# Kernel optimization log

Hardware: AMD Instinct MI355X
Metric: run time of the kernel (lower is better)

## Reference

```python
import jax, jax.numpy as jnp
import numpy as np

EMBED_DIM = 1024
NUM_HEADS = 8
HEAD_DIM = EMBED_DIM // NUM_HEADS


def setup_inputs() -> dict:
    key = jax.random.key(0)
    k1, k2, k3, k4, k5 = jax.random.split(key, 5)
    B, N, D = 4, 2048, EMBED_DIM
    scale = 1.0 / np.sqrt(D)
    return {
        "representation": jax.random.normal(k1, (B, N, D), dtype=jnp.float32),
        "W_qkv": jax.random.normal(k2, (D, 3 * D), dtype=jnp.float32) * scale,
        "b_qkv": jnp.zeros((3 * D,), dtype=jnp.float32),
        "W_proj": jax.random.normal(k3, (D, D), dtype=jnp.float32) * scale,
        "b_proj": jnp.zeros((D,), dtype=jnp.float32),
    }


def reference(representation, W_qkv, b_qkv, W_proj, b_proj):
    B, N, D = representation.shape
    H, Hd = NUM_HEADS, HEAD_DIM
    qkv = jnp.einsum("bnd,de->bne", representation, W_qkv) + b_qkv  # [B,N,3D]
    q, k, v = jnp.split(qkv, 3, axis=-1)
    # [B,N,D] -> [B,H,N,Hd]
    split_heads = lambda x: x.reshape(B, N, H, Hd).transpose(0, 2, 1, 3)
    q, k, v = split_heads(q), split_heads(k), split_heads(v)
    dots = jnp.einsum("bhqd,bhkd->bhqk", q, k) * (Hd ** -0.5)  # [B,H,N,N]
    attn = jax.nn.softmax(dots, axis=-1)
    out = jnp.einsum("bhqk,bhkd->bhqd", attn, v)
    out = out.transpose(0, 2, 1, 3).reshape(B, N, D)  # merge heads
    return jnp.einsum("bnd,de->bne", out, W_proj) + b_proj
```

## Files before the change

### kernel.cpp

```cpp
#include <hip/hip_runtime.h>
#include <hip/hip_bf16.h>
#include <cstdint>

typedef unsigned short u16;
typedef __attribute__((ext_vector_type(8))) short short8;
typedef __attribute__((ext_vector_type(4))) float f32x4;
typedef __attribute__((ext_vector_type(4))) unsigned short u16x4;

#define NSEQ 2048
#define DMODEL 1024
#define NH 8
#define HD 128
#define KDIM 1024
#define SCALE 0.08838834764831845f

__device__ __forceinline__ u16 f2b(float f) {
  __hip_bfloat16 h = __float2bfloat16(f);
  union { __hip_bfloat16 h; u16 u; } cv; cv.h = h; return cv.u;
}
__device__ __forceinline__ f32x4 zero4() { f32x4 z = {0.f, 0.f, 0.f, 0.f}; return z; }

__device__ __forceinline__ void gload_lds16(const u16* g, u16* l) {
  __builtin_amdgcn_global_load_lds(
      (__attribute__((address_space(1))) void*)g,
      (__attribute__((address_space(3))) void*)l, 16, 0, 0);
}

__global__ void cvt_f32_bf16(const float* __restrict__ in, u16* __restrict__ out) {
  const size_t i = ((size_t)blockIdx.x * 256 + threadIdx.x) * 8;
  f32x4 a = *(const f32x4*)&in[i];
  f32x4 b = *(const f32x4*)&in[i + 4];
  short8 o;
#pragma unroll
  for (int j = 0; j < 4; ++j) { o[j] = (short)f2b(a[j]); o[4 + j] = (short)f2b(b[j]); }
  *(short8*)&out[i] = o;
}

__global__ void transpose_k(const float* __restrict__ in, u16* __restrict__ out,
                            int R, int C) {
  __shared__ u16 tile[32][33];
  const int tx = threadIdx.x, ty = threadIdx.y;
  const int c = blockIdx.x * 32 + tx;
  const int r0 = blockIdx.y * 32;
  for (int i = ty; i < 32; i += 8) tile[i][tx] = f2b(in[(size_t)(r0 + i) * C + c]);
  __syncthreads();
  const int oc = r0 + tx;
  const int c0 = blockIdx.x * 32;
  for (int i = ty; i < 32; i += 8) out[(size_t)(c0 + i) * R + oc] = tile[tx][i];
}

template <int MODE>
__global__ __launch_bounds__(256, 2) void gemm128(
    const u16* __restrict__ A, const u16* __restrict__ Bt,
    const float* __restrict__ bias, u16* __restrict__ o0,
    u16* __restrict__ o1, u16* __restrict__ o2, float* __restrict__ of) {
  __shared__ __align__(16) u16 sA[128 * 64];
  __shared__ __align__(16) u16 sB[128 * 64];

  const int tid = threadIdx.x;
  const int lane = tid & 63;
  const int w = tid >> 6;
  const int quad = lane >> 4, ln = lane & 15;
  const int m0 = blockIdx.y * 128, n0 = blockIdx.x * 128;
  const int wm = (w >> 1) * 64, wn = (w & 1) * 64;

  f32x4 acc[4][4];
#pragma unroll
  for (int i = 0; i < 4; ++i)
#pragma unroll
    for (int j = 0; j < 4; ++j) acc[i][j] = zero4();

  const int cbase = w * 4;
  for (int kb = 0; kb < KDIM / 64; ++kb) {
    __syncthreads();
    const int k0 = kb * 64;
#pragma unroll
    for (int i = 0; i < 4; ++i) {
      int c = (cbase + i) * 64 + lane;
      int r = c >> 3, s = c & 7;
      gload_lds16(A + (size_t)(m0 + r) * KDIM + k0 + s * 8, &sA[(cbase + i) * 512]);
      gload_lds16(Bt + (size_t)(n0 + r) * KDIM + k0 + s * 8, &sB[(cbase + i) * 512]);
    }
    __syncthreads();
#pragma unroll
    for (int ks = 0; ks < 2; ++ks) {
      short8 af[4], bf[4];
      const int kc = ks * 4 + quad;
#pragma unroll
      for (int t = 0; t < 4; ++t) {
        af[t] = *(const short8*)&sA[(wm + t * 16 + ln) * 64 + kc * 8];
        bf[t] = *(const short8*)&sB[(wn + t * 16 + ln) * 64 + kc * 8];
      }
#pragma unroll
      for (int mt = 0; mt < 4; ++mt)
#pragma unroll
        for (int nt = 0; nt < 4; ++nt)
          acc[mt][nt] = __builtin_amdgcn_mfma_f32_16x16x32_bf16(
              af[mt], bf[nt], acc[mt][nt], 0, 0, 0);
    }
  }

  if (MODE == 0) {
    const int which = n0 >> 10;
    const int h = (n0 & 1023) >> 7;
#pragma unroll
    for (int mt = 0; mt < 4; ++mt) {
      const int rbase = m0 + wm + mt * 16 + quad * 4;
      const int b = rbase >> 11;
      const int n = rbase & 2047;
#pragma unroll
      for (int nt = 0; nt < 4; ++nt) {
        const int dcol = wn + nt * 16 + ln;
        const float bv = bias[n0 + dcol];
        if (which == 0) {
          u16* p = o0 + ((size_t)(b * NH + h) * NSEQ + n) * HD + dcol;
#pragma unroll
          for (int rr = 0; rr < 4; ++rr)
            p[(size_t)rr * HD] = f2b((acc[mt][nt][rr] + bv) * SCALE);
        } else if (which == 1) {
          u16* p = o1 + ((size_t)(b * NH + h) * NSEQ + n) * HD + dcol;
#pragma unroll
          for (int rr = 0; rr < 4; ++rr)
            p[(size_t)rr * HD] = f2b(acc[mt][nt][rr] + bv);
        } else {
          u16x4 pk;
#pragma unroll
          for (int rr = 0; rr < 4; ++rr) pk[rr] = f2b(acc[mt][nt][rr] + bv);
          *(u16x4*)&o2[((size_t)(b * NH + h) * HD + dcol) * NSEQ + n] = pk;
        }
      }
    }
  } else {
#pragma unroll
    for (int mt = 0; mt < 4; ++mt) {
      const int rbase = m0 + wm + mt * 16 + quad * 4;
#pragma unroll
      for (int nt = 0; nt < 4; ++nt) {
        const int col = n0 + wn + nt * 16 + ln;
        const float bv = bias[col];
#pragma unroll
        for (int rr = 0; rr < 4; ++rr)
          of[(size_t)(rbase + rr) * DMODEL + col] = acc[mt][nt][rr] + bv;
      }
    }
  }
}

__global__ __launch_bounds__(256, 2) void attn_fused(
    const u16* __restrict__ Q, const u16* __restrict__ K,
    const u16* __restrict__ Vt, u16* __restrict__ AO) {
  __shared__ __align__(16) u16 sK[64 * 136];
  __shared__ __align__(16) u16 sV[128 * 72];
  __shared__ __align__(16) u16 sP[128 * 72];

  const int tid = threadIdx.x;
  const int w = tid >> 6, lane = tid & 63;
  const int quad = lane >> 4, ln = lane & 15;
  const int bh = blockIdx.y;
  const int q0 = blockIdx.x * 128;

  const u16* Qb = Q + ((size_t)bh * NSEQ + q0) * HD;
  const u16* Kb = K + (size_t)bh * NSEQ * HD;
  const u16* Vb = Vt + (size_t)bh * HD * NSEQ;

  short8 qf[2][4];
#pragma unroll
  for (int mt = 0; mt < 2; ++mt)
#pragma unroll
    for (int ks = 0; ks < 4; ++ks)
      qf[mt][ks] = *(const short8*)&Qb[(size_t)(w * 32 + mt * 16 + ln) * HD +
                                       ks * 32 + quad * 8];

  f32x4 o[2][8];
#pragma unroll
  for (int mt = 0; mt < 2; ++mt)
#pragma unroll
    for (int dt = 0; dt < 8; ++dt) o[mt][dt] = zero4();
  float m_st[2][4], l_st[2][4];
#pragma unroll
  for (int mt = 0; mt < 2; ++mt)
#pragma unroll
    for (int rr = 0; rr < 4; ++rr) { m_st[mt][rr] = -1e30f; l_st[mt][rr] = 0.f; }

  short8 kreg[4], vreg[4];
#pragma unroll
  for (int i = 0; i < 4; ++i) {
    int c = i * 256 + tid;
    int rk = c >> 4, sk = c & 15;
    kreg[i] = *(const short8*)&Kb[(size_t)rk * HD + sk * 8];
    int rv = c >> 3, sv = c & 7;
    vreg[i] = *(const short8*)&Vb[(size_t)rv * NSEQ + sv * 8];
  }

  for (int kv = 0; kv < NSEQ; kv += 64) {
    __syncthreads();
#pragma unroll
    for (int i = 0; i < 4; ++i) {
      int c = i * 256 + tid;
      int rk = c >> 4, sk = c & 15;
      *(short8*)&sK[rk * 136 + sk * 8] = kreg[i];
      int rv = c >> 3, sv = c & 7;
      *(short8*)&sV[rv * 72 + sv * 8] = vreg[i];
    }
    __syncthreads();

    if (kv + 64 < NSEQ) {
#pragma unroll
      for (int i = 0; i < 4; ++i) {
        int c = i * 256 + tid;
        int rk = c >> 4, sk = c & 15;
        kreg[i] = *(const short8*)&Kb[(size_t)(kv + 64 + rk) * HD + sk * 8];
        int rv = c >> 3, sv = c & 7;
        vreg[i] = *(const short8*)&Vb[(size_t)rv * NSEQ + kv + 64 + sv * 8];
      }
    }

    f32x4 sacc[2][4];
#pragma unroll
    for (int mt = 0; mt < 2; ++mt)
#pragma unroll
      for (int nt = 0; nt < 4; ++nt) sacc[mt][nt] = zero4();
#pragma unroll
    for (int ks = 0; ks < 4; ++ks) {
      short8 kf[4];
#pragma unroll
      for (int nt = 0; nt < 4; ++nt)
        kf[nt] = *(const short8*)&sK[(nt * 16 + ln) * 136 + ks * 32 + quad * 8];
#pragma unroll
      for (int mt = 0; mt < 2; ++mt)
#pragma unroll
        for (int nt = 0; nt < 4; ++nt)
          sacc[mt][nt] = __builtin_amdgcn_mfma_f32_16x16x32_bf16(
              qf[mt][ks], kf[nt], sacc[mt][nt], 0, 0, 0);
    }

#pragma unroll
    for (int mt = 0; mt < 2; ++mt) {
      float mnew[4], alpha[4], rsum[4];
#pragma unroll
      for (int rr = 0; rr < 4; ++rr) {
        float v = fmaxf(fmaxf(sacc[mt][0][rr], sacc[mt][1][rr]),
                        fmaxf(sacc[mt][2][rr], sacc[mt][3][rr]));
#pragma unroll
        for (int off = 8; off >= 1; off >>= 1) v = fmaxf(v, __shfl_xor(v, off, 64));
        mnew[rr] = fmaxf(m_st[mt][rr], v);
        alpha[rr] = __expf(m_st[mt][rr] - mnew[rr]);
        m_st[mt][rr] = mnew[rr];
        rsum[rr] = 0.f;
      }
#pragma unroll
      for (int nt = 0; nt < 4; ++nt)
#pragma unroll
        for (int rr = 0; rr < 4; ++rr) {
          float p = __expf(sacc[mt][nt][rr] - mnew[rr]);
          rsum[rr] += p;
          sP[(w * 32 + mt * 16 + quad * 4 + rr) * 72 + nt * 16 + ln] = f2b(p);
        }
#pragma unroll
      for (int rr = 0; rr < 4; ++rr) {
        float v = rsum[rr];
#pragma unroll
        for (int off = 8; off >= 1; off >>= 1) v += __shfl_xor(v, off, 64);
        l_st[mt][rr] = l_st[mt][rr] * alpha[rr] + v;
      }
#pragma unroll
      for (int dt = 0; dt < 8; ++dt)
#pragma unroll
        for (int rr = 0; rr < 4; ++rr) o[mt][dt][rr] *= alpha[rr];
    }

#pragma unroll
    for (int ks2 = 0; ks2 < 2; ++ks2) {
      short8 pf[2], vf[8];
#pragma unroll
      for (int mt = 0; mt < 2; ++mt)
        pf[mt] = *(const short8*)&sP[(w * 32 + mt * 16 + ln) * 72 +
                                     ks2 * 32 + quad * 8];
#pragma unroll
      for (int dt = 0; dt < 8; ++dt)
        vf[dt] = *(const short8*)&sV[(dt * 16 + ln) * 72 + ks2 * 32 + quad * 8];
#pragma unroll
      for (int mt = 0; mt < 2; ++mt)
#pragma unroll
        for (int dt = 0; dt < 8; ++dt)
          o[mt][dt] = __builtin_amdgcn_mfma_f32_16x16x32_bf16(
              pf[mt], vf[dt], o[mt][dt], 0, 0, 0);
    }
  }

  const int b = bh >> 3, h = bh & 7;
#pragma unroll
  for (int mt = 0; mt < 2; ++mt) {
    float inv[4];
#pragma unroll
    for (int rr = 0; rr < 4; ++rr) inv[rr] = 1.0f / fmaxf(l_st[mt][rr], 1e-30f);
    const int rbase = q0 + w * 32 + mt * 16 + quad * 4;
#pragma unroll
    for (int dt = 0; dt < 8; ++dt) {
      const int d = dt * 16 + ln;
#pragma unroll
      for (int rr = 0; rr < 4; ++rr)
        AO[((size_t)b * NSEQ + rbase + rr) * DMODEL + h * HD + d] =
            f2b(o[mt][dt][rr] * inv[rr]);
    }
  }
}

extern "C" void kernel_launch(void* const* d_in, const int* in_sizes, int n_in,
                              void* d_out, int out_size, void* d_ws, size_t ws_size,
                              hipStream_t stream) {
  const float* X = (const float*)d_in[0];
  const float* Wqkv = (const float*)d_in[1];
  const float* bqkv = (const float*)d_in[2];
  const float* Wproj = (const float*)d_in[3];
  const float* bproj = (const float*)d_in[4];
  float* out = (float*)d_out;

  const size_t NEED_BYTES =
      2ull * (8388608  + 3072 * 1024 + 1024 * 1024 + 3 * 8388608 + 8388608);
  if (ws_size < NEED_BYTES) return;

  u16* ws = (u16*)d_ws;
  u16* Xb = ws;
  u16* WqkvT = Xb + 8388608;
  u16* WprojT = WqkvT + 3072 * 1024;
  u16* Qb = WprojT + 1024 * 1024;
  u16* Kb = Qb + 8388608;
  u16* Vtb = Kb + 8388608;
  u16* AO = Vtb + 8388608;

  cvt_f32_bf16<<<8388608 / (256 * 8), 256, 0, stream>>>(X, Xb);
  transpose_k<<<dim3(3072 / 32, 1024 / 32), dim3(32, 8), 0, stream>>>(Wqkv, WqkvT, 1024, 3072);
  transpose_k<<<dim3(1024 / 32, 1024 / 32), dim3(32, 8), 0, stream>>>(Wproj, WprojT, 1024, 1024);
  gemm128<0><<<dim3(3072 / 128, 8192 / 128), 256, 0, stream>>>(
      Xb, WqkvT, bqkv, Qb, Kb, Vtb, nullptr);
  attn_fused<<<dim3(2048 / 128, 32), 256, 0, stream>>>(Qb, Kb, Vtb, AO);
  gemm128<1><<<dim3(1024 / 128, 8192 / 128), 256, 0, stream>>>(
      AO, WprojT, bproj, nullptr, nullptr, nullptr, out);
}
```

Measured before the change: 332.4 us.

## Load K/V tiles directly to LDS with swizzle, alias K and P buffers

Replaces the register-staged K/V prefetch with direct global-to-LDS loads using an XOR swizzle instead of row padding. K and P now share one LDS buffer, with an extra barrier after QK^T, so the kernel uses less shared memory and fewer registers, and launch bounds are raised to three blocks per CU. The log2(e) factor is also folded into the Q scale so that exp2f can replace __expf. The cost is losing software prefetch overlap of the next tile and adding a third barrier per iteration.

New measurement: 434.6 us. 30.7% more time.

```diff
diff --git a/kernel.cpp b/kernel.cpp
--- a/kernel.cpp
+++ b/kernel.cpp
@@ -12,7 +12,7 @@
 #define NH 8
 #define HD 128
 #define KDIM 1024
-#define SCALE 0.08838834764831845f
+#define QSCALE (0.08838834764831845f * 1.4426950408889634f)
 
 __device__ __forceinline__ u16 f2b(float f) {
   __hip_bfloat16 h = __float2bfloat16(f);
@@ -116,7 +116,7 @@
           u16* p = o0 + ((size_t)(b * NH + h) * NSEQ + n) * HD + dcol;
 #pragma unroll
           for (int rr = 0; rr < 4; ++rr)
-            p[(size_t)rr * HD] = f2b((acc[mt][nt][rr] + bv) * SCALE);
+            p[(size_t)rr * HD] = f2b((acc[mt][nt][rr] + bv) * QSCALE);
         } else if (which == 1) {
           u16* p = o1 + ((size_t)(b * NH + h) * NSEQ + n) * HD + dcol;
 #pragma unroll
@@ -146,12 +146,13 @@
   }
 }
 
-__global__ __launch_bounds__(256, 2) void attn_fused(
+__global__ __launch_bounds__(256, 3) void attn_fused(
     const u16* __restrict__ Q, const u16* __restrict__ K,
     const u16* __restrict__ Vt, u16* __restrict__ AO) {
-  __shared__ __align__(16) u16 sK[64 * 136];
-  __shared__ __align__(16) u16 sV[128 * 72];
-  __shared__ __align__(16) u16 sP[128 * 72];
+  __shared__ __align__(16) u16 sKP[128 * 72];
+  __shared__ __align__(16) u16 sV[128 * 64];
+  u16* sK = sKP;
+  u16* sP = sKP;
 
   const int tid = threadIdx.x;
   const int w = tid >> 6, lane = tid & 63;
@@ -182,38 +183,18 @@
 #pragma unroll
     for (int rr = 0; rr < 4; ++rr) { m_st[mt][rr] = -1e30f; l_st[mt][rr] = 0.f; }
 
-  short8 kreg[4], vreg[4];
-#pragma unroll
-  for (int i = 0; i < 4; ++i) {
-    int c = i * 256 + tid;
-    int rk = c >> 4, sk = c & 15;
-    kreg[i] = *(const short8*)&Kb[(size_t)rk * HD + sk * 8];
-    int rv = c >> 3, sv = c & 7;
-    vreg[i] = *(const short8*)&Vb[(size_t)rv * NSEQ + sv * 8];
-  }
-
+  const int cbase = w * 4;
   for (int kv = 0; kv < NSEQ; kv += 64) {
     __syncthreads();
 #pragma unroll
     for (int i = 0; i < 4; ++i) {
-      int c = i * 256 + tid;
-      int rk = c >> 4, sk = c & 15;
-      *(short8*)&sK[rk * 136 + sk * 8] = kreg[i];
-      int rv = c >> 3, sv = c & 7;
-      *(short8*)&sV[rv * 72 + sv * 8] = vreg[i];
-    }
-    __syncthreads();
-
-    if (kv + 64 < NSEQ) {
-#pragma unroll
-      for (int i = 0; i < 4; ++i) {
-        int c = i * 256 + tid;
-        int rk = c >> 4, sk = c & 15;
-        kreg[i] = *(const short8*)&Kb[(size_t)(kv + 64 + rk) * HD + sk * 8];
-        int rv = c >> 3, sv = c & 7;
-        vreg[i] = *(const short8*)&Vb[(size_t)rv * NSEQ + kv + 64 + sv * 8];
-      }
-    }
+      int c = (cbase + i) * 64 + lane;
+      int rk = c >> 4, sk = c & 15, gk = sk ^ (rk & 15);
+      gload_lds16(Kb + (size_t)(kv + rk) * HD + gk * 8, &sK[(cbase + i) * 512]);
+      int rv = c >> 3, sv = c & 7, gv = sv ^ (rv & 7);
+      gload_lds16(Vb + (size_t)rv * NSEQ + kv + gv * 8, &sV[(cbase + i) * 512]);
+    }
+    __syncthreads();
 
     f32x4 sacc[2][4];
 #pragma unroll
@@ -223,9 +204,10 @@
 #pragma unroll
     for (int ks = 0; ks < 4; ++ks) {
       short8 kf[4];
+      const int kc = ks * 4 + quad;
 #pragma unroll
       for (int nt = 0; nt < 4; ++nt)
-        kf[nt] = *(const short8*)&sK[(nt * 16 + ln) * 136 + ks * 32 + quad * 8];
+        kf[nt] = *(const short8*)&sK[(nt * 16 + ln) * 128 + (kc ^ ln) * 8];
 #pragma unroll
       for (int mt = 0; mt < 2; ++mt)
 #pragma unroll
@@ -233,6 +215,7 @@
           sacc[mt][nt] = __builtin_amdgcn_mfma_f32_16x16x32_bf16(
               qf[mt][ks], kf[nt], sacc[mt][nt], 0, 0, 0);
     }
+    __syncthreads();
 
 #pragma unroll
     for (int mt = 0; mt < 2; ++mt) {
@@ -244,7 +227,7 @@
 #pragma unroll
         for (int off = 8; off >= 1; off >>= 1) v = fmaxf(v, __shfl_xor(v, off, 64));
         mnew[rr] = fmaxf(m_st[mt][rr], v);
-        alpha[rr] = __expf(m_st[mt][rr] - mnew[rr]);
+        alpha[rr] = exp2f(m_st[mt][rr] - mnew[rr]);
         m_st[mt][rr] = mnew[rr];
         rsum[rr] = 0.f;
       }
@@ -252,7 +235,7 @@
       for (int nt = 0; nt < 4; ++nt)
 #pragma unroll
         for (int rr = 0; rr < 4; ++rr) {
-          float p = __expf(sacc[mt][nt][rr] - mnew[rr]);
+          float p = exp2f(sacc[mt][nt][rr] - mnew[rr]);
           rsum[rr] += p;
           sP[(w * 32 + mt * 16 + quad * 4 + rr) * 72 + nt * 16 + ln] = f2b(p);
         }
@@ -272,13 +255,14 @@
 #pragma unroll
     for (int ks2 = 0; ks2 < 2; ++ks2) {
       short8 pf[2], vf[8];
+      const int kc2 = ks2 * 4 + quad;
 #pragma unroll
       for (int mt = 0; mt < 2; ++mt)
         pf[mt] = *(const short8*)&sP[(w * 32 + mt * 16 + ln) * 72 +
                                      ks2 * 32 + quad * 8];
 #pragma unroll
       for (int dt = 0; dt < 8; ++dt)
-        vf[dt] = *(const short8*)&sV[(dt * 16 + ln) * 72 + ks2 * 32 + quad * 8];
+        vf[dt] = *(const short8*)&sV[(dt * 16 + ln) * 64 + (kc2 ^ (ln & 7)) * 8];
 #pragma unroll
       for (int mt = 0; mt < 2; ++mt)
 #pragma unroll
```

## Use 8 waves of 16 query rows in attention and fold log2e into Q scale

Applied to the files above, without the earlier changes.

The attention kernel moves from 256 threads (4 waves × 32 query rows) to 512 threads (8 waves × 16 query rows) per 128-row block. This halves per-thread registers and K/V staging loads and raises wave-level parallelism. Log2(e) is folded into the Q scaling in the QKV GEMM epilogue so the softmax can use exp2f instead of __expf. The trade-off is that each K/V fragment read from LDS now feeds half as many MFMAs, so LDS read traffic per unit of work roughly doubles.

Measured after the change: 335.6 us. Within noise of the previous version (+1.0%).

```diff
diff --git a/kernel.cpp b/kernel.cpp
--- a/kernel.cpp
+++ b/kernel.cpp
@@ -12,7 +12,7 @@
 #define NH 8
 #define HD 128
 #define KDIM 1024
-#define SCALE 0.08838834764831845f
+#define QSCALE (0.08838834764831845f * 1.4426950408889634f)
 
 __device__ __forceinline__ u16 f2b(float f) {
   __hip_bfloat16 h = __float2bfloat16(f);
@@ -116,7 +116,7 @@
           u16* p = o0 + ((size_t)(b * NH + h) * NSEQ + n) * HD + dcol;
 #pragma unroll
           for (int rr = 0; rr < 4; ++rr)
-            p[(size_t)rr * HD] = f2b((acc[mt][nt][rr] + bv) * SCALE);
+            p[(size_t)rr * HD] = f2b((acc[mt][nt][rr] + bv) * QSCALE);
         } else if (which == 1) {
           u16* p = o1 + ((size_t)(b * NH + h) * NSEQ + n) * HD + dcol;
 #pragma unroll
@@ -146,7 +146,7 @@
   }
 }
 
-__global__ __launch_bounds__(256, 2) void attn_fused(
+__global__ __launch_bounds__(512, 4) void attn_fused(
     const u16* __restrict__ Q, const u16* __restrict__ K,
     const u16* __restrict__ Vt, u16* __restrict__ AO) {
   __shared__ __align__(16) u16 sK[64 * 136];
@@ -163,29 +163,22 @@
   const u16* Kb = K + (size_t)bh * NSEQ * HD;
   const u16* Vb = Vt + (size_t)bh * HD * NSEQ;
 
-  short8 qf[2][4];
-#pragma unroll
-  for (int mt = 0; mt < 2; ++mt)
-#pragma unroll
-    for (int ks = 0; ks < 4; ++ks)
-      qf[mt][ks] = *(const short8*)&Qb[(size_t)(w * 32 + mt * 16 + ln) * HD +
-                                       ks * 32 + quad * 8];
-
-  f32x4 o[2][8];
-#pragma unroll
-  for (int mt = 0; mt < 2; ++mt)
-#pragma unroll
-    for (int dt = 0; dt < 8; ++dt) o[mt][dt] = zero4();
-  float m_st[2][4], l_st[2][4];
-#pragma unroll
-  for (int mt = 0; mt < 2; ++mt)
-#pragma unroll
-    for (int rr = 0; rr < 4; ++rr) { m_st[mt][rr] = -1e30f; l_st[mt][rr] = 0.f; }
-
-  short8 kreg[4], vreg[4];
-#pragma unroll
-  for (int i = 0; i < 4; ++i) {
-    int c = i * 256 + tid;
+  short8 qf[4];
+#pragma unroll
+  for (int ks = 0; ks < 4; ++ks)
+    qf[ks] = *(const short8*)&Qb[(size_t)(w * 16 + ln) * HD + ks * 32 + quad * 8];
+
+  f32x4 o[8];
+#pragma unroll
+  for (int dt = 0; dt < 8; ++dt) o[dt] = zero4();
+  float m_st[4], l_st[4];
+#pragma unroll
+  for (int rr = 0; rr < 4; ++rr) { m_st[rr] = -1e30f; l_st[rr] = 0.f; }
+
+  short8 kreg[2], vreg[2];
+#pragma unroll
+  for (int i = 0; i < 2; ++i) {
+    int c = i * 512 + tid;
     int rk = c >> 4, sk = c & 15;
     kreg[i] = *(const short8*)&Kb[(size_t)rk * HD + sk * 8];
     int rv = c >> 3, sv = c & 7;
@@ -195,8 +188,8 @@
   for (int kv = 0; kv < NSEQ; kv += 64) {
     __syncthreads();
 #pragma unroll
-    for (int i = 0; i < 4; ++i) {
-      int c = i * 256 + tid;
+    for (int i = 0; i < 2; ++i) {
+      int c = i * 512 + tid;
       int rk = c >> 4, sk = c & 15;
       *(short8*)&sK[rk * 136 + sk * 8] = kreg[i];
       int rv = c >> 3, sv = c & 7;
@@ -206,8 +199,8 @@
 
     if (kv + 64 < NSEQ) {
 #pragma unroll
-      for (int i = 0; i < 4; ++i) {
-        int c = i * 256 + tid;
+      for (int i = 0; i < 2; ++i) {
+        int c = i * 512 + tid;
         int rk = c >> 4, sk = c & 15;
         kreg[i] = *(const short8*)&Kb[(size_t)(kv + 64 + rk) * HD + sk * 8];
         int rv = c >> 3, sv = c & 7;
@@ -215,11 +208,9 @@
       }
     }
 
-    f32x4 sacc[2][4];
-#pragma unroll
-    for (int mt = 0; mt < 2; ++mt)
-#pragma unroll
-      for (int nt = 0; nt < 4; ++nt) sacc[mt][nt] = zero4();
+    f32x4 sacc[4];
+#pragma unroll
+    for (int nt = 0; nt < 4; ++nt) sacc[nt] = zero4();
 #pragma unroll
     for (int ks = 0; ks < 4; ++ks) {
       short8 kf[4];
@@ -227,81 +218,71 @@
       for (int nt = 0; nt < 4; ++nt)
         kf[nt] = *(const short8*)&sK[(nt * 16 + ln) * 136 + ks * 32 + quad * 8];
 #pragma unroll
-      for (int mt = 0; mt < 2; ++mt)
-#pragma unroll
-        for (int nt = 0; nt < 4; ++nt)
-          sacc[mt][nt] = __builtin_amdgcn_mfma_f32_16x16x32_bf16(
-              qf[mt][ks], kf[nt], sacc[mt][nt], 0, 0, 0);
-    }
-
-#pragma unroll
-    for (int mt = 0; mt < 2; ++mt) {
+      for (int nt = 0; nt < 4; ++nt)
+        sacc[nt] = __builtin_amdgcn_mfma_f32_16x16x32_bf16(
+            qf[ks], kf[nt], sacc[nt], 0, 0, 0);
+    }
+
+    {
       float mnew[4], alpha[4], rsum[4];
 #pragma unroll
       for (int rr = 0; rr < 4; ++rr) {
-        float v = fmaxf(fmaxf(sacc[mt][0][rr], sacc[mt][1][rr]),
-                        fmaxf(sacc[mt][2][rr], sacc[mt][3][rr]));
+        float v = fmaxf(fmaxf(sacc[0][rr], sacc[1][rr]),
+                        fmaxf(sacc[2][rr], sacc[3][rr]));
 #pragma unroll
         for (int off = 8; off >= 1; off >>= 1) v = fmaxf(v, __shfl_xor(v, off, 64));
-        mnew[rr] = fmaxf(m_st[mt][rr], v);
-        alpha[rr] = __expf(m_st[mt][rr] - mnew[rr]);
-        m_st[mt][rr] = mnew[rr];
+        mnew[rr] = fmaxf(m_st[rr], v);
+        alpha[rr] = exp2f(m_st[rr] - mnew[rr]);
+        m_st[rr] = mnew[rr];
         rsum[rr] = 0.f;
       }
 #pragma unroll
       for (int nt = 0; nt < 4; ++nt)
 #pragma unroll
         for (int rr = 0; rr < 4; ++rr) {
-          float p = __expf(sacc[mt][nt][rr] - mnew[rr]);
+          float p = exp2f(sacc[nt][rr] - mnew[rr]);
           rsum[rr] += p;
-          sP[(w * 32 + mt * 16 + quad * 4 + rr) * 72 + nt * 16 + ln] = f2b(p);
+          sP[(w * 16 + quad * 4 + rr) * 72 + nt * 16 + ln] = f2b(p);
         }
 #pragma unroll
       for (int rr = 0; rr < 4; ++rr) {
         float v = rsum[rr];
 #pragma unroll
         for (int off = 8; off >= 1; off >>= 1) v += __shfl_xor(v, off, 64);
-        l_st[mt][rr] = l_st[mt][rr] * alpha[rr] + v;
+        l_st[rr] = l_st[rr] * alpha[rr] + v;
       }
 #pragma unroll
       for (int dt = 0; dt < 8; ++dt)
 #pragma unroll
-        for (int rr = 0; rr < 4; ++rr) o[mt][dt][rr] *= alpha[rr];
+        for (int rr = 0; rr < 4; ++rr) o[dt][rr] *= alpha[rr];
     }
 
 #pragma unroll
     for (int ks2 = 0; ks2 < 2; ++ks2) {
-      short8 pf[2], vf[8];
-#pragma unroll
-      for (int mt = 0; mt < 2; ++mt)
-        pf[mt] = *(const short8*)&sP[(w * 32 + mt * 16 + ln) * 72 +
-                                     ks2 * 32 + quad * 8];
+      short8 pf, vf[8];
+      pf = *(const short8*)&sP[(w * 16 + ln) * 72 + ks2 * 32 + quad * 8];
 #pragma unroll
       for (int dt = 0; dt < 8; ++dt)
         vf[dt] = *(const short8*)&sV[(dt * 16 + ln) * 72 + ks2 * 32 + quad * 8];
 #pragma unroll
-      for (int mt = 0; mt < 2; ++mt)
-#pragma unroll
-        for (int dt = 0; dt < 8; ++dt)
-          o[mt][dt] = __builtin_amdgcn_mfma_f32_16x16x32_bf16(
-              pf[mt], vf[dt], o[mt][dt], 0, 0, 0);
+      for (int dt = 0; dt < 8; ++dt)
+        o[dt] = __builtin_amdgcn_mfma_f32_16x16x32_bf16(pf, vf[dt], o[dt], 0, 0, 0);
     }
   }
 
   const int b = bh >> 3, h = bh & 7;
-#pragma unroll
-  for (int mt = 0; mt < 2; ++mt) {
+  {
     float inv[4];
 #pragma unroll
-    for (int rr = 0; rr < 4; ++rr) inv[rr] = 1.0f / fmaxf(l_st[mt][rr], 1e-30f);
-    const int rbase = q0 + w * 32 + mt * 16 + quad * 4;
+    for (int rr = 0; rr < 4; ++rr) inv[rr] = 1.0f / fmaxf(l_st[rr], 1e-30f);
+    const int rbase = q0 + w * 16 + quad * 4;
 #pragma unroll
     for (int dt = 0; dt < 8; ++dt) {
       const int d = dt * 16 + ln;
 #pragma unroll
       for (int rr = 0; rr < 4; ++rr)
         AO[((size_t)b * NSEQ + rbase + rr) * DMODEL + h * HD + d] =
-            f2b(o[mt][dt][rr] * inv[rr]);
+            f2b(o[dt][rr] * inv[rr]);
     }
   }
 }
@@ -334,7 +315,7 @@
   transpose_k<<<dim3(1024 / 32, 1024 / 32), dim3(32, 8), 0, stream>>>(Wproj, WprojT, 1024, 1024);
   gemm128<0><<<dim3(3072 / 128, 8192 / 128), 256, 0, stream>>>(
       Xb, WqkvT, bqkv, Qb, Kb, Vtb, nullptr);
-  attn_fused<<<dim3(2048 / 128, 32), 256, 0, stream>>>(Qb, Kb, Vtb, AO);
+  attn_fused<<<dim3(2048 / 128, 32), 512, 0, stream>>>(Qb, Kb, Vtb, AO);
   gemm128<1><<<dim3(1024 / 128, 8192 / 128), 256, 0, stream>>>(
       AO, WprojT, bproj, nullptr, nullptr, nullptr, out);
 }
```
